# Kernel optimization log

Hardware: AMD Instinct MI355X
Metric: run time of the kernel (lower is better)

The kernel has to match this reference:

```python
import jax, jax.numpy as jnp
import numpy as np

NUM_HEADS = 8
WS = 2  # window_size


def setup_inputs() -> dict:
    key = jax.random.key(0)
    k1, k2, k3 = jax.random.split(key, 3)
    B, N, C = 8, 4096, 512
    x = jax.random.normal(k1, (B, N, C), dtype=jnp.float32)
    W_qkv = jax.random.normal(k2, (3 * C, C), dtype=jnp.float32) * 0.02  # nn.Linear weight [out,in], no bias
    W_proj = jax.random.normal(k3, (C, C), dtype=jnp.float32) * 0.02
    b_proj = jnp.zeros((C,), dtype=jnp.float32)
    return {"x": x, "W_qkv": W_qkv, "W_proj": W_proj, "b_proj": b_proj}


def _attn(q, k, v, scale):
    # q,k,v: [..., heads, T, hd]
    logits = jnp.einsum('...qd,...kd->...qk', q, k) * scale
    p = jax.nn.softmax(logits, axis=-1)
    return jnp.einsum('...qk,...kd->...qd', p, v)


def reference(x, W_qkv, W_proj, b_proj):
    B, N, C = x.shape
    H = W = int(N ** 0.5)
    nh, hd = NUM_HEADS, C // NUM_HEADS
    scale = hd ** -0.5

    # ---- hi branch: avg-pool then global attention on pooled tokens ----
    x_img = x.reshape(B, H, W, C)
    x_hi = x_img.reshape(B, H // WS, WS, W // WS, WS, C).mean(axis=(2, 4))  # [B,Hh,Wh,C]
    Hh, Wh = H // WS, W // WS
    N_hi = Hh * Wh
    x_hi = x_hi.reshape(B, N_hi, C)

    qkv_hi = (x_hi @ W_qkv.T).reshape(B, N_hi, 3, nh, hd).transpose(2, 0, 3, 1, 4)
    out_hi = _attn(qkv_hi[0], qkv_hi[1], qkv_hi[2], scale)          # [B,nh,N_hi,hd]
    out_hi = out_hi.transpose(0, 2, 1, 3).reshape(B, N_hi, C)

    # bilinear upsample (align_corners=False == half-pixel, matches jax.image.resize)
    hi_img = out_hi.reshape(B, Hh, Wh, C).transpose(0, 3, 1, 2)      # [B,C,Hh,Wh]
    hi_up = jax.image.resize(hi_img, (B, C, H, W), method='bilinear')
    out_hi = hi_up.reshape(B, C, N).transpose(0, 2, 1)               # [B,N,C]

    # ---- lo branch: windowed attention (replicating torch unfold layout) ----
    # torch: x.unfold(1,ws,ws).unfold(2,ws,ws) -> [B,Hh,Wh,C,ws,ws]; then
    # .reshape(B,-1,ws*ws,C) reinterprets the contiguous [C,ws,ws] block as [ws*ws,C].
    wnd = x_img.reshape(B, Hh, WS, Wh, WS, C).transpose(0, 1, 3, 5, 2, 4)  # [B,Hh,Wh,C,ws,ws]
    nW = Hh * Wh
    T = WS * WS
    windows = wnd.reshape(B, nW, T, C)  # same raw-memory reinterpretation as torch

    qkv_lo = (windows @ W_qkv.T).reshape(B, nW, T, 3, nh, hd).transpose(3, 0, 1, 4, 2, 5)
    out_lo = _attn(qkv_lo[0], qkv_lo[1], qkv_lo[2], scale)           # [B,nW,nh,T,hd]
    out_lo = out_lo.transpose(0, 1, 3, 2, 4).reshape(B, nW, T, C)

    out_lo = out_lo.reshape(B, Hh, Wh, WS, WS, C).transpose(0, 1, 3, 2, 4, 5).reshape(B, N, C)

    out = out_hi + out_lo
    out = out @ W_proj.T + b_proj
    return out
```

## Files before the change

### kernel.cpp

```cpp
#include <hip/hip_runtime.h>
#include <stdint.h>

typedef unsigned short u16b;
typedef short s16x8 __attribute__((ext_vector_type(8)));
typedef unsigned short u16x4 __attribute__((ext_vector_type(4)));
typedef float f32x4 __attribute__((ext_vector_type(4)));

__device__ __forceinline__ u16b f2bf(float f) {
    uint32_t u = __float_as_uint(f);
    uint32_t r = (u + 0x7FFFu + ((u >> 16) & 1u)) >> 16;
    return (u16b)r;
}
__device__ __forceinline__ u16b f2bf_fast(float f) {
    return (u16b)((__float_as_uint(f) + 0x8000u) >> 16);
}
__device__ __forceinline__ float bf2f(u16b h) {
    return __uint_as_float(((uint32_t)h) << 16);
}

typedef const __attribute__((address_space(1))) void* gas_ptr;
typedef __attribute__((address_space(3))) void* las_ptr;
__device__ __forceinline__ void gload_lds16(const void* g, void* l) {
    __builtin_amdgcn_global_load_lds((gas_ptr)g, (las_ptr)l, 16, 0, 0);
}

__global__ void cast_weights(const float* __restrict__ wqkv, const float* __restrict__ wproj,
                             u16b* __restrict__ wqkv_bf, u16b* __restrict__ wproj_bf) {
    int i = blockIdx.x * 256 + threadIdx.x;
    if (i < 1536 * 512) wqkv_bf[i] = f2bf(wqkv[i]);
    if (i < 512 * 512) wproj_bf[i] = f2bf(wproj[i]);
}

__global__ __launch_bounds__(256) void pool_pack(const float* __restrict__ x,
                                                 u16b* __restrict__ x_hi,
                                                 u16b* __restrict__ xw) {
    int i = blockIdx.x * 256 + threadIdx.x;
    int c4 = i & 127;
    int t = i >> 7;
    int wj = t & 31, wi = (t >> 5) & 31, b = t >> 10;
    const float* p00 = x + ((size_t)b * 4096 + (size_t)(wi * 2) * 64 + wj * 2) * 512 + c4 * 4;
    f32x4 v00 = *(const f32x4*)p00;
    f32x4 v01 = *(const f32x4*)(p00 + 512);
    f32x4 v10 = *(const f32x4*)(p00 + 64 * 512);
    f32x4 v11 = *(const f32x4*)(p00 + 65 * 512);

    u16b ph[4];
#pragma unroll
    for (int j = 0; j < 4; ++j)
        ph[j] = f2bf((v00[j] + v01[j] + v10[j] + v11[j]) * 0.25f);
    *(u16x4*)(x_hi + (size_t)t * 512 + c4 * 4) = *(u16x4*)ph;

    u16b pk[16];
#pragma unroll
    for (int j = 0; j < 4; ++j) {
        pk[j * 4 + 0] = f2bf(v00[j]);
        pk[j * 4 + 1] = f2bf(v01[j]);
        pk[j * 4 + 2] = f2bf(v10[j]);
        pk[j * 4 + 3] = f2bf(v11[j]);
    }
    u16b* dst = xw + ((size_t)t * 4 + (c4 >> 5)) * 512 + (c4 & 31) * 16;
    *(s16x8*)dst = *(s16x8*)pk;
    *(s16x8*)(dst + 8) = *(s16x8*)(pk + 8);
}


template <int RT>
__device__ __forceinline__ void stage_region(const u16b* gsrc, int K, u16b* lds,
                                             int wv, int ldrow, int ldk) {
#pragma unroll
    for (int j = 0; j < 2; ++j) {
        int c = j * 8 + wv;
        int chunk;
        if (RT == 0)      chunk = c + ((c >> 3) << 3);
        else if (RT == 1) chunk = c + ((c >> 3) << 3) + 8;
        else if (RT == 2) chunk = ((c >> 2) << 3) + (c & 3);
        else              chunk = ((c >> 2) << 3) + (c & 3) + 4;
        gload_lds16(gsrc + (size_t)(chunk * 8 + ldrow) * K + ldk, lds + chunk * 512);
    }
}

template <int MH, int NH, int LA, int LB>
__device__ __forceinline__ void ds_quad(const u16b* Asb, const u16b* Bsb,
                                        int gm, int gn, int l15, int fsw0, int fsw1,
                                        s16x8 (&af)[4][2], s16x8 (&bf)[2][2]) {
    if (LA) {
#pragma unroll
        for (int i = 0; i < 4; ++i) {
            const u16b* p = Asb + (gm * 128 + (MH * 4 + i) * 16 + l15) * 64;
            af[i][0] = *(const s16x8*)(p + fsw0);
            af[i][1] = *(const s16x8*)(p + fsw1);
        }
    }
    if (LB) {
#pragma unroll
        for (int i = 0; i < 2; ++i) {
            const u16b* p = Bsb + (gn * 64 + (NH * 2 + i) * 16 + l15) * 64;
            bf[i][0] = *(const s16x8*)(p + fsw0);
            bf[i][1] = *(const s16x8*)(p + fsw1);
        }
    }
}

template <int MH, int NH>
__device__ __forceinline__ void mfma_quad(s16x8 (&af)[4][2], s16x8 (&bf)[2][2], f32x4 (&acc)[8][4]) {
    __builtin_amdgcn_s_setprio(1);
#pragma unroll
    for (int ks = 0; ks < 2; ++ks)
#pragma unroll
        for (int i = 0; i < 4; ++i)
#pragma unroll
            for (int j = 0; j < 2; ++j)
                acc[MH * 4 + i][NH * 2 + j] = __builtin_amdgcn_mfma_f32_16x16x32_bf16(
                    af[i][ks], bf[j][ks], acc[MH * 4 + i][NH * 2 + j], 0, 0, 0);
    __builtin_amdgcn_s_setprio(0);
}

template <int OUT_F32>
__global__ __launch_bounds__(512, 2) void gemm8(const u16b* __restrict__ A, const u16b* __restrict__ Bt,
                                                u16b* __restrict__ Cbf, float* __restrict__ Cf,
                                                const float* __restrict__ bias, int M, int Nn, int K,
                                                int NB) {
    __shared__ u16b As[2][256 * 64];
    __shared__ u16b Bs[2][256 * 64];
    int tid = threadIdx.x;
    int wv = tid >> 6, lane = tid & 63;
    int quad = lane >> 4, l15 = lane & 15;
    int gm = wv >> 2, gn = wv & 3;

    int nwg = gridDim.x, bid = blockIdx.x;
    int swz = (bid & 7) * (nwg >> 3) + (bid >> 3);
    int nb = swz % NB, mb = swz / NB;
    int m0 = mb * 256, n0 = nb * 256;
    const u16b* Ap = A + (size_t)m0 * K;
    const u16b* Btp = Bt + (size_t)n0 * K;

    int ldrow = lane >> 3;
    int ldk = ((lane & 7) ^ ldrow) * 8;
    int fsw0 = (quad ^ (l15 & 7)) * 8;
    int fsw1 = ((4 + quad) ^ (l15 & 7)) * 8;

    f32x4 acc[8][4] = {};
    s16x8 af[4][2], bf[2][2];
    int nt = K >> 6;

#pragma unroll
    for (int r = 0; r < 4; ++r) {
        int chunk = r * 8 + wv;
        gload_lds16(Ap + (size_t)(chunk * 8 + ldrow) * K + ldk, &As[0][0] + chunk * 512);
    }
#pragma unroll
    for (int r = 0; r < 4; ++r) {
        int chunk = r * 8 + wv;
        gload_lds16(Btp + (size_t)(chunk * 8 + ldrow) * K + ldk, &Bs[0][0] + chunk * 512);
    }
    stage_region<0>(Ap + 64, K, &As[1][0], wv, ldrow, ldk);
    stage_region<3>(Btp + 64, K, &Bs[1][0], wv, ldrow, ldk);
    asm volatile("s_waitcnt vmcnt(4)" ::: "memory");
    __builtin_amdgcn_s_barrier();

    for (int t0 = 0; t0 < nt; t0 += 2) {
        bool s2 = (t0 + 2) < nt;
        bool s3 = (t0 + 3) < nt;
        ds_quad<0, 0, 1, 1>(&As[0][0], &Bs[0][0], gm, gn, l15, fsw0, fsw1, af, bf);
        stage_region<1>(Ap + (size_t)(t0 + 1) * 64, K, &As[1][0], wv, ldrow, ldk);
        __builtin_amdgcn_s_barrier();
        mfma_quad<0, 0>(af, bf, acc);
        __builtin_amdgcn_s_barrier();
        ds_quad<0, 1, 0, 1>(&As[0][0], &Bs[0][0], gm, gn, l15, fsw0, fsw1, af, bf);
        stage_region<2>(Btp + (size_t)(t0 + 1) * 64, K, &Bs[1][0], wv, ldrow, ldk);
        __builtin_amdgcn_s_barrier();
        mfma_quad<0, 1>(af, bf, acc);
        __builtin_amdgcn_s_barrier();
        ds_quad<1, 1, 1, 0>(&As[0][0], &Bs[0][0], gm, gn, l15, fsw0, fsw1, af, bf);
        if (s2) stage_region<0>(Ap + (size_t)(t0 + 2) * 64, K, &As[0][0], wv, ldrow, ldk);
        __builtin_amdgcn_s_barrier();
        mfma_quad<1, 1>(af, bf, acc);
        __builtin_amdgcn_s_barrier();
        ds_quad<1, 0, 0, 1>(&As[0][0], &Bs[0][0], gm, gn, l15, fsw0, fsw1, af, bf);
        if (s2) stage_region<3>(Btp + (size_t)(t0 + 2) * 64, K, &Bs[0][0], wv, ldrow, ldk);
        __builtin_amdgcn_s_barrier();
        mfma_quad<1, 0>(af, bf, acc);
        if (s2) { asm volatile("s_waitcnt vmcnt(4)" ::: "memory"); }
        else    { asm volatile("s_waitcnt vmcnt(0)" ::: "memory"); }
        __builtin_amdgcn_s_barrier();
        ds_quad<0, 0, 1, 1>(&As[1][0], &Bs[1][0], gm, gn, l15, fsw0, fsw1, af, bf);
        if (s2) stage_region<1>(Ap + (size_t)(t0 + 2) * 64, K, &As[0][0], wv, ldrow, ldk);
        __builtin_amdgcn_s_barrier();
        mfma_quad<0, 0>(af, bf, acc);
        __builtin_amdgcn_s_barrier();
        ds_quad<0, 1, 0, 1>(&As[1][0], &Bs[1][0], gm, gn, l15, fsw0, fsw1, af, bf);
        if (s2) stage_region<2>(Btp + (size_t)(t0 + 2) * 64, K, &Bs[0][0], wv, ldrow, ldk);
        __builtin_amdgcn_s_barrier();
        mfma_quad<0, 1>(af, bf, acc);
        __builtin_amdgcn_s_barrier();
        ds_quad<1, 1, 1, 0>(&As[1][0], &Bs[1][0], gm, gn, l15, fsw0, fsw1, af, bf);
        if (s3) stage_region<0>(Ap + (size_t)(t0 + 3) * 64, K, &As[1][0], wv, ldrow, ldk);
        __builtin_amdgcn_s_barrier();
        mfma_quad<1, 1>(af, bf, acc);
        __builtin_amdgcn_s_barrier();
        ds_quad<1, 0, 0, 1>(&As[1][0], &Bs[1][0], gm, gn, l15, fsw0, fsw1, af, bf);
        if (s3) stage_region<3>(Btp + (size_t)(t0 + 3) * 64, K, &Bs[1][0], wv, ldrow, ldk);
        __builtin_amdgcn_s_barrier();
        mfma_quad<1, 0>(af, bf, acc);
        if (s3) { asm volatile("s_waitcnt vmcnt(4)" ::: "memory"); }
        else    { asm volatile("s_waitcnt vmcnt(0)" ::: "memory"); }
        __builtin_amdgcn_s_barrier();
    }

#pragma unroll
    for (int mi = 0; mi < 8; ++mi)
#pragma unroll
        for (int ni = 0; ni < 4; ++ni) {
            int row = m0 + gm * 128 + mi * 16 + quad * 4;
            int col = n0 + gn * 64 + ni * 16 + l15;
            if (OUT_F32) {
                float bv = bias[col];
#pragma unroll
                for (int r = 0; r < 4; ++r)
                    Cf[(size_t)(row + r) * Nn + col] = acc[mi][ni][r] + bv;
            } else {
#pragma unroll
                for (int r = 0; r < 4; ++r)
                    Cbf[(size_t)(row + r) * Nn + col] = f2bf(acc[mi][ni][r]);
            }
        }
}

__global__ __launch_bounds__(256) void transpose_v(const u16b* __restrict__ qkv, u16b* __restrict__ vt) {
    __shared__ u16b tile[64 * 72];
    int bh = blockIdx.y, nt = blockIdx.x;
    int b = bh >> 3, h = bh & 7;
    int tid = threadIdx.x;
    int row = tid >> 2, part = tid & 3;
    const u16b* src = qkv + ((size_t)b * 1024 + nt * 64 + row) * 1536 + 1024 + h * 64 + part * 16;
    *(s16x8*)&tile[row * 72 + part * 16] = *(const s16x8*)src;
    *(s16x8*)&tile[row * 72 + part * 16 + 8] = *(const s16x8*)(src + 8);
    __syncthreads();
    u16b* dst = vt + ((size_t)bh * 64 + row) * 1024 + nt * 64 + part * 16;
#pragma unroll
    for (int j = 0; j < 16; ++j) dst[j] = tile[(part * 16 + j) * 72 + row];
}

__global__ __launch_bounds__(256) void attn_hi(const u16b* __restrict__ qkv,
                                               const u16b* __restrict__ vt,
                                               u16b* __restrict__ out_hi) {
    __shared__ u16b Ks[2][64 * 64];
    __shared__ u16b Vs[2][64 * 64];
    __shared__ u16b P[4][16 * 64];
    int tid = threadIdx.x, wave = tid >> 6, lane = tid & 63;
    int quad = lane >> 4, l15 = lane & 15;
    int bh = blockIdx.x;
    int qb = blockIdx.y;
    int b = bh >> 3, h = bh & 7;
    int qr0 = qb * 64 + wave * 16;

    const size_t qkv_b = (size_t)b * 1024 * 1536;
    const u16b* kg = qkv + qkv_b + 512 + h * 64;
    const u16b* vg = vt + (size_t)bh * 64 * 1024;

    int srow8 = lane >> 3;
    int ssw = ((lane & 7) ^ srow8) * 8;
    int fsw0 = (quad ^ (l15 & 7)) * 8;
    int fsw1 = ((4 + quad) ^ (l15 & 7)) * 8;

    s16x8 qf[2];
    qf[0] = *(const s16x8*)(qkv + qkv_b + (size_t)(qr0 + l15) * 1536 + h * 64 + quad * 8);
    qf[1] = *(const s16x8*)(qkv + qkv_b + (size_t)(qr0 + l15) * 1536 + h * 64 + 32 + quad * 8);

#pragma unroll
    for (int i = 0; i < 2; ++i) {
        int chunk = wave * 2 + i;
        int row = chunk * 8 + srow8;
        gload_lds16(kg + (size_t)row * 1536 + ssw, (u16b*)Ks[0] + chunk * 512);
        gload_lds16(vg + (size_t)row * 1024 + ssw, (u16b*)Vs[0] + chunk * 512);
    }

    f32x4 o[4] = {};
    f32x4 ls = {0.f, 0.f, 0.f, 0.f};
    u16b* pl = P[wave];
    const float c_scale = 0.18033688011f;

    for (int kb = 0; kb < 16; ++kb) {
        int cur = kb & 1, nxt = cur ^ 1;
        __syncthreads();
        if (kb < 15) {
#pragma unroll
            for (int i = 0; i < 2; ++i) {
                int chunk = wave * 2 + i;
                int row = chunk * 8 + srow8;
                gload_lds16(kg + (size_t)((kb + 1) * 64 + row) * 1536 + ssw, (u16b*)Ks[nxt] + chunk * 512);
                gload_lds16(vg + (size_t)row * 1024 + (kb + 1) * 64 + ssw, (u16b*)Vs[nxt] + chunk * 512);
            }
        }
        const u16b* Kc = Ks[cur];
        const u16b* Vc = Vs[cur];

        f32x4 s[4] = {};
#pragma unroll
        for (int nt = 0; nt < 4; ++nt) {
            s16x8 kf0 = *(const s16x8*)(Kc + (nt * 16 + l15) * 64 + fsw0);
            s16x8 kf1 = *(const s16x8*)(Kc + (nt * 16 + l15) * 64 + fsw1);
            s[nt] = __builtin_amdgcn_mfma_f32_16x16x32_bf16(qf[0], kf0, s[nt], 0, 0, 0);
            s[nt] = __builtin_amdgcn_mfma_f32_16x16x32_bf16(qf[1], kf1, s[nt], 0, 0, 0);
        }
#pragma unroll
        for (int nt = 0; nt < 4; ++nt) {
            f32x4 p;
#pragma unroll
            for (int r = 0; r < 4; ++r) p[r] = exp2f(s[nt][r] * c_scale);
            ls += p;
#pragma unroll
            for (int r = 0; r < 4; ++r) {
                int prow = quad * 4 + r;
                int slc = (nt * 2 + (l15 >> 3)) ^ (prow & 7);
                pl[prow * 64 + slc * 8 + (l15 & 7)] = f2bf_fast(p[r]);
            }
        }
        s16x8 pa0 = *(const s16x8*)(pl + l15 * 64 + fsw0);
        s16x8 pa1 = *(const s16x8*)(pl + l15 * 64 + fsw1);
#pragma unroll
        for (int nd = 0; nd < 4; ++nd) {
            s16x8 vf0 = *(const s16x8*)(Vc + (nd * 16 + l15) * 64 + fsw0);
            s16x8 vf1 = *(const s16x8*)(Vc + (nd * 16 + l15) * 64 + fsw1);
            o[nd] = __builtin_amdgcn_mfma_f32_16x16x32_bf16(pa0, vf0, o[nd], 0, 0, 0);
            o[nd] = __builtin_amdgcn_mfma_f32_16x16x32_bf16(pa1, vf1, o[nd], 0, 0, 0);
        }
    }

    float rs[4];
#pragma unroll
    for (int r = 0; r < 4; ++r) {
        float t = ls[r];
#pragma unroll
        for (int msk = 1; msk < 16; msk <<= 1) t += __shfl_xor(t, msk);
        rs[r] = 1.f / t;
    }
#pragma unroll
    for (int nd = 0; nd < 4; ++nd)
#pragma unroll
        for (int r = 0; r < 4; ++r) {
            int row = qr0 + quad * 4 + r;
            int col = h * 64 + nd * 16 + l15;
            out_hi[((size_t)b * 1024 + row) * 512 + col] = f2bf(o[nd][r] * rs[r]);
        }
}

__global__ __launch_bounds__(256) void attn_lo_up(const u16b* __restrict__ qkv_lo,
                                                  const u16b* __restrict__ out_hi,
                                                  u16b* __restrict__ attn_sum) {
    __shared__ float P[4][64];
    int tid = threadIdx.x, wave = tid >> 6, lane = tid & 63;
    int quad = lane >> 4, l15 = lane & 15;
    int wg = blockIdx.x * 4 + wave;
    int h = wg & 7, w4 = (wg >> 3) & 255, b = wg >> 11;
    int w0 = w4 * 4;

    const u16b* qb = qkv_lo + ((size_t)(b * 1024 + w0 + (l15 >> 2)) * 4 + (l15 & 3)) * 1536 + h * 64 + quad * 8;
    s16x8 qf0 = *(const s16x8*)qb;
    s16x8 qf1 = *(const s16x8*)(qb + 32);
    s16x8 kf0 = *(const s16x8*)(qb + 512);
    s16x8 kf1 = *(const s16x8*)(qb + 544);
    f32x4 s = {};
    s = __builtin_amdgcn_mfma_f32_16x16x32_bf16(qf0, kf0, s, 0, 0, 0);
    s = __builtin_amdgcn_mfma_f32_16x16x32_bf16(qf1, kf1, s, 0, 0, 0);
    bool valid = (l15 >> 2) == quad;
    float* pl = &P[wave][quad * 16];
#pragma unroll
    for (int r = 0; r < 4; ++r) {
        float v = s[r] * 0.125f;
        float m = fmaxf(v, __shfl_xor(v, 1));
        m = fmaxf(m, __shfl_xor(m, 2));
        float e = exp2f((v - m) * 1.44269504f);
        float sm = e + __shfl_xor(e, 1);
        sm += __shfl_xor(sm, 2);
        if (valid) pl[r * 4 + (l15 & 3)] = e / sm;
    }

    int win = quad, d4 = l15 * 4;
    int w = w0 + win;
    int wi = w >> 5, wj = w & 31;
    const u16b* vb = qkv_lo + ((size_t)(b * 1024 + w) * 4) * 1536 + 1024 + h * 64 + d4;
    float vf[4][4];
#pragma unroll
    for (int tk = 0; tk < 4; ++tk) {
        u16x4 vv = *(const u16x4*)(vb + (size_t)tk * 1536);
#pragma unroll
        for (int j = 0; j < 4; ++j) vf[tk][j] = bf2f(vv[j]);
    }
    int rr[3] = { wi > 0 ? wi - 1 : 0, wi, wi < 31 ? wi + 1 : 31 };
    int cc[3] = { wj > 0 ? wj - 1 : 0, wj, wj < 31 ? wj + 1 : 31 };
    float hv[3][3][4];
    const u16b* hb = out_hi + (size_t)b * 1024 * 512 + h * 64 + d4;
#pragma unroll
    for (int iy = 0; iy < 3; ++iy)
#pragma unroll
        for (int ix = 0; ix < 3; ++ix) {
            u16x4 t = *(const u16x4*)(hb + (size_t)(rr[iy] * 32 + cc[ix]) * 512);
#pragma unroll
            for (int j = 0; j < 4; ++j) hv[iy][ix][j] = bf2f(t[j]);
        }
#pragma unroll
    for (int tq = 0; tq < 4; ++tq) {
        f32x4 pq = *(const f32x4*)&P[wave][win * 16 + tq * 4];
        int py = tq >> 1, px = tq & 1;
        float wy0 = py ? 0.75f : 0.25f, wx0 = px ? 0.75f : 0.25f;
        float wy1 = 1.f - wy0, wx1 = 1.f - wx0;
        u16b ov[4];
#pragma unroll
        for (int j = 0; j < 4; ++j) {
            float o = pq[0] * vf[0][j] + pq[1] * vf[1][j] + pq[2] * vf[2][j] + pq[3] * vf[3][j];
            float vu = wy0 * (wx0 * hv[py][px][j] + wx1 * hv[py][px + 1][j])
                     + wy1 * (wx0 * hv[py + 1][px][j] + wx1 * hv[py + 1][px + 1][j]);
            ov[j] = f2bf(o + vu);
        }
        int n = (wi * 2 + py) * 64 + wj * 2 + px;
        *(u16x4*)(attn_sum + ((size_t)(b * 4096 + n)) * 512 + h * 64 + d4) = *(u16x4*)ov;
    }
}

extern "C" void kernel_launch(void* const* d_in, const int* in_sizes, int n_in,
                              void* d_out, int out_size, void* d_ws, size_t ws_size,
                              hipStream_t stream) {
    (void)in_sizes; (void)n_in; (void)out_size; (void)ws_size;
    const float* x = (const float*)d_in[0];
    const float* Wqkv = (const float*)d_in[1];
    const float* Wproj = (const float*)d_in[2];
    const float* bproj = (const float*)d_in[3];
    float* out = (float*)d_out;

    char* ws = (char*)d_ws;
    size_t off = 0;
    auto alloc = [&](size_t bytes) { void* p = ws + off; off += bytes; return p; };
    u16b* wqkv_bf = (u16b*)alloc((size_t)1536 * 512 * 2);
    u16b* wproj_bf = (u16b*)alloc((size_t)512 * 512 * 2);
    u16b* x_hi    = (u16b*)alloc((size_t)8 * 1024 * 512 * 2);
    u16b* xw      = (u16b*)alloc((size_t)8 * 1024 * 4 * 512 * 2);
    u16b* qkv_hi  = (u16b*)alloc((size_t)8 * 1024 * 1536 * 2);
    u16b* qkv_lo  = (u16b*)alloc((size_t)8 * 4096 * 1536 * 2);
    u16b* vt      = (u16b*)alloc((size_t)64 * 64 * 1024 * 2);
    u16b* out_hi  = (u16b*)alloc((size_t)8 * 1024 * 512 * 2);
    u16b* attn_sum= (u16b*)alloc((size_t)8 * 4096 * 512 * 2);

    cast_weights<<<dim3(3072), dim3(256), 0, stream>>>(Wqkv, Wproj, wqkv_bf, wproj_bf);
    pool_pack<<<dim3(4096), dim3(256), 0, stream>>>(x, x_hi, xw);
    gemm8<0><<<dim3(192), dim3(512), 0, stream>>>(x_hi, wqkv_bf, qkv_hi, nullptr, nullptr, 8192, 1536, 512, 6);
    gemm8<0><<<dim3(768), dim3(512), 0, stream>>>(xw, wqkv_bf, qkv_lo, nullptr, nullptr, 32768, 1536, 512, 6);
    transpose_v<<<dim3(16, 64), dim3(256), 0, stream>>>(qkv_hi, vt);
    attn_hi<<<dim3(64, 16), dim3(256), 0, stream>>>(qkv_hi, vt, out_hi);
    attn_lo_up<<<dim3(4096), dim3(256), 0, stream>>>(qkv_lo, out_hi, attn_sum);
    gemm8<1><<<dim3(256), dim3(512), 0, stream>>>(attn_sum, wproj_bf, nullptr, out, bproj, 32768, 512, 512, 2);
}
```

Baseline: 313.0 us.

## Double query rows per wave in attn_hi and merge the two QKV GEMMs

attn_hi now handles 32 query rows per wave (128 per block), so each K/V tile loaded into LDS serves twice as many MFMAs, and the grid is halved. Workspace buffers are reordered so xw and x_hi, and likewise qkv_lo and qkv_hi, sit next to each other. This lets a single GEMM launch over 40960 rows produce both QKV outputs, removing one launch and the tail of the smaller GEMM. In exchange attn_hi uses more registers and LDS per block (occupancy hint of 3), and the merged GEMM depends on the buffers staying contiguous.

```diff
diff --git a/kernel.cpp b/kernel.cpp
--- a/kernel.cpp
+++ b/kernel.cpp
@@ -241,18 +241,18 @@
     for (int j = 0; j < 16; ++j) dst[j] = tile[(part * 16 + j) * 72 + row];
 }
 
-__global__ __launch_bounds__(256) void attn_hi(const u16b* __restrict__ qkv,
-                                               const u16b* __restrict__ vt,
-                                               u16b* __restrict__ out_hi) {
+__global__ __launch_bounds__(256, 3) void attn_hi(const u16b* __restrict__ qkv,
+                                                  const u16b* __restrict__ vt,
+                                                  u16b* __restrict__ out_hi) {
     __shared__ u16b Ks[2][64 * 64];
     __shared__ u16b Vs[2][64 * 64];
-    __shared__ u16b P[4][16 * 64];
+    __shared__ u16b P[4][32 * 64];
     int tid = threadIdx.x, wave = tid >> 6, lane = tid & 63;
     int quad = lane >> 4, l15 = lane & 15;
     int bh = blockIdx.x;
     int qb = blockIdx.y;
     int b = bh >> 3, h = bh & 7;
-    int qr0 = qb * 64 + wave * 16;
+    int qr0 = qb * 128 + wave * 32;
 
     const size_t qkv_b = (size_t)b * 1024 * 1536;
     const u16b* kg = qkv + qkv_b + 512 + h * 64;
@@ -263,9 +263,13 @@
     int fsw0 = (quad ^ (l15 & 7)) * 8;
     int fsw1 = ((4 + quad) ^ (l15 & 7)) * 8;
 
-    s16x8 qf[2];
-    qf[0] = *(const s16x8*)(qkv + qkv_b + (size_t)(qr0 + l15) * 1536 + h * 64 + quad * 8);
-    qf[1] = *(const s16x8*)(qkv + qkv_b + (size_t)(qr0 + l15) * 1536 + h * 64 + 32 + quad * 8);
+    s16x8 qf[2][2];
+#pragma unroll
+    for (int qh = 0; qh < 2; ++qh) {
+        const u16b* qp = qkv + qkv_b + (size_t)(qr0 + qh * 16 + l15) * 1536 + h * 64 + quad * 8;
+        qf[qh][0] = *(const s16x8*)qp;
+        qf[qh][1] = *(const s16x8*)(qp + 32);
+    }
 
 #pragma unroll
     for (int i = 0; i < 2; ++i) {
@@ -275,8 +279,8 @@
         gload_lds16(vg + (size_t)row * 1024 + ssw, (u16b*)Vs[0] + chunk * 512);
     }
 
-    f32x4 o[4] = {};
-    f32x4 ls = {0.f, 0.f, 0.f, 0.f};
+    f32x4 o[2][4] = {};
+    f32x4 ls[2] = {};
     u16b* pl = P[wave];
     const float c_scale = 0.18033688011f;
 
@@ -295,54 +299,67 @@
         const u16b* Kc = Ks[cur];
         const u16b* Vc = Vs[cur];
 
-        f32x4 s[4] = {};
+        f32x4 s[2][4] = {};
 #pragma unroll
         for (int nt = 0; nt < 4; ++nt) {
             s16x8 kf0 = *(const s16x8*)(Kc + (nt * 16 + l15) * 64 + fsw0);
             s16x8 kf1 = *(const s16x8*)(Kc + (nt * 16 + l15) * 64 + fsw1);
-            s[nt] = __builtin_amdgcn_mfma_f32_16x16x32_bf16(qf[0], kf0, s[nt], 0, 0, 0);
-            s[nt] = __builtin_amdgcn_mfma_f32_16x16x32_bf16(qf[1], kf1, s[nt], 0, 0, 0);
-        }
-#pragma unroll
-        for (int nt = 0; nt < 4; ++nt) {
-            f32x4 p;
-#pragma unroll
-            for (int r = 0; r < 4; ++r) p[r] = exp2f(s[nt][r] * c_scale);
-            ls += p;
-#pragma unroll
-            for (int r = 0; r < 4; ++r) {
-                int prow = quad * 4 + r;
-                int slc = (nt * 2 + (l15 >> 3)) ^ (prow & 7);
-                pl[prow * 64 + slc * 8 + (l15 & 7)] = f2bf_fast(p[r]);
+            s[0][nt] = __builtin_amdgcn_mfma_f32_16x16x32_bf16(qf[0][0], kf0, s[0][nt], 0, 0, 0);
+            s[0][nt] = __builtin_amdgcn_mfma_f32_16x16x32_bf16(qf[0][1], kf1, s[0][nt], 0, 0, 0);
+            s[1][nt] = __builtin_amdgcn_mfma_f32_16x16x32_bf16(qf[1][0], kf0, s[1][nt], 0, 0, 0);
+            s[1][nt] = __builtin_amdgcn_mfma_f32_16x16x32_bf16(qf[1][1], kf1, s[1][nt], 0, 0, 0);
+        }
+#pragma unroll
+        for (int qh = 0; qh < 2; ++qh)
+#pragma unroll
+            for (int nt = 0; nt < 4; ++nt) {
+                f32x4 p;
+#pragma unroll
+                for (int r = 0; r < 4; ++r) p[r] = exp2f(s[qh][nt][r] * c_scale);
+                ls[qh] += p;
+#pragma unroll
+                for (int r = 0; r < 4; ++r) {
+                    int prow = qh * 16 + quad * 4 + r;
+                    int slc = (nt * 2 + (l15 >> 3)) ^ (prow & 7);
+                    pl[prow * 64 + slc * 8 + (l15 & 7)] = f2bf_fast(p[r]);
+                }
             }
-        }
-        s16x8 pa0 = *(const s16x8*)(pl + l15 * 64 + fsw0);
-        s16x8 pa1 = *(const s16x8*)(pl + l15 * 64 + fsw1);
+        s16x8 pa[2][2];
+#pragma unroll
+        for (int qh = 0; qh < 2; ++qh) {
+            pa[qh][0] = *(const s16x8*)(pl + (qh * 16 + l15) * 64 + fsw0);
+            pa[qh][1] = *(const s16x8*)(pl + (qh * 16 + l15) * 64 + fsw1);
+        }
 #pragma unroll
         for (int nd = 0; nd < 4; ++nd) {
             s16x8 vf0 = *(const s16x8*)(Vc + (nd * 16 + l15) * 64 + fsw0);
             s16x8 vf1 = *(const s16x8*)(Vc + (nd * 16 + l15) * 64 + fsw1);
-            o[nd] = __builtin_amdgcn_mfma_f32_16x16x32_bf16(pa0, vf0, o[nd], 0, 0, 0);
-            o[nd] = __builtin_amdgcn_mfma_f32_16x16x32_bf16(pa1, vf1, o[nd], 0, 0, 0);
-        }
-    }
-
-    float rs[4];
-#pragma unroll
-    for (int r = 0; r < 4; ++r) {
-        float t = ls[r];
-#pragma unroll
-        for (int msk = 1; msk < 16; msk <<= 1) t += __shfl_xor(t, msk);
-        rs[r] = 1.f / t;
-    }
-#pragma unroll
-    for (int nd = 0; nd < 4; ++nd)
+            o[0][nd] = __builtin_amdgcn_mfma_f32_16x16x32_bf16(pa[0][0], vf0, o[0][nd], 0, 0, 0);
+            o[0][nd] = __builtin_amdgcn_mfma_f32_16x16x32_bf16(pa[0][1], vf1, o[0][nd], 0, 0, 0);
+            o[1][nd] = __builtin_amdgcn_mfma_f32_16x16x32_bf16(pa[1][0], vf0, o[1][nd], 0, 0, 0);
+            o[1][nd] = __builtin_amdgcn_mfma_f32_16x16x32_bf16(pa[1][1], vf1, o[1][nd], 0, 0, 0);
+        }
+    }
+
+#pragma unroll
+    for (int qh = 0; qh < 2; ++qh) {
+        float rs[4];
 #pragma unroll
         for (int r = 0; r < 4; ++r) {
-            int row = qr0 + quad * 4 + r;
-            int col = h * 64 + nd * 16 + l15;
-            out_hi[((size_t)b * 1024 + row) * 512 + col] = f2bf(o[nd][r] * rs[r]);
-        }
+            float t = ls[qh][r];
+#pragma unroll
+            for (int msk = 1; msk < 16; msk <<= 1) t += __shfl_xor(t, msk);
+            rs[r] = 1.f / t;
+        }
+#pragma unroll
+        for (int nd = 0; nd < 4; ++nd)
+#pragma unroll
+            for (int r = 0; r < 4; ++r) {
+                int row = qr0 + qh * 16 + quad * 4 + r;
+                int col = h * 64 + nd * 16 + l15;
+                out_hi[((size_t)b * 1024 + row) * 512 + col] = f2bf(o[qh][nd][r] * rs[r]);
+            }
+    }
 }
 
 __global__ __launch_bounds__(256) void attn_lo_up(const u16b* __restrict__ qkv_lo,
@@ -433,20 +450,19 @@
     auto alloc = [&](size_t bytes) { void* p = ws + off; off += bytes; return p; };
     u16b* wqkv_bf = (u16b*)alloc((size_t)1536 * 512 * 2);
     u16b* wproj_bf = (u16b*)alloc((size_t)512 * 512 * 2);
+    u16b* xw      = (u16b*)alloc((size_t)8 * 1024 * 4 * 512 * 2);
     u16b* x_hi    = (u16b*)alloc((size_t)8 * 1024 * 512 * 2);
-    u16b* xw      = (u16b*)alloc((size_t)8 * 1024 * 4 * 512 * 2);
+    u16b* qkv_lo  = (u16b*)alloc((size_t)8 * 4096 * 1536 * 2);
     u16b* qkv_hi  = (u16b*)alloc((size_t)8 * 1024 * 1536 * 2);
-    u16b* qkv_lo  = (u16b*)alloc((size_t)8 * 4096 * 1536 * 2);
     u16b* vt      = (u16b*)alloc((size_t)64 * 64 * 1024 * 2);
     u16b* out_hi  = (u16b*)alloc((size_t)8 * 1024 * 512 * 2);
     u16b* attn_sum= (u16b*)alloc((size_t)8 * 4096 * 512 * 2);
 
     cast_weights<<<dim3(3072), dim3(256), 0, stream>>>(Wqkv, Wproj, wqkv_bf, wproj_bf);
     pool_pack<<<dim3(4096), dim3(256), 0, stream>>>(x, x_hi, xw);
-    gemm8<0><<<dim3(192), dim3(512), 0, stream>>>(x_hi, wqkv_bf, qkv_hi, nullptr, nullptr, 8192, 1536, 512, 6);
-    gemm8<0><<<dim3(768), dim3(512), 0, stream>>>(xw, wqkv_bf, qkv_lo, nullptr, nullptr, 32768, 1536, 512, 6);
+    gemm8<0><<<dim3(960), dim3(512), 0, stream>>>(xw, wqkv_bf, qkv_lo, nullptr, nullptr, 40960, 1536, 512, 6);
     transpose_v<<<dim3(16, 64), dim3(256), 0, stream>>>(qkv_hi, vt);
-    attn_hi<<<dim3(64, 16), dim3(256), 0, stream>>>(qkv_hi, vt, out_hi);
+    attn_hi<<<dim3(64, 8), dim3(256), 0, stream>>>(qkv_hi, vt, out_hi);
     attn_lo_up<<<dim3(4096), dim3(256), 0, stream>>>(qkv_lo, out_hi, attn_sum);
     gemm8<1><<<dim3(256), dim3(512), 0, stream>>>(attn_sum, wproj_bf, nullptr, out, bproj, 32768, 512, 512, 2);
 }
```

Result: no change. 314.2 us (+0.4%).
